# Kernel tuning notes

Hardware: AMD Instinct MI355X
Metric: run time of the kernel (lower is better)

Reference implementation:

```python
import jax, jax.numpy as jnp
import numpy as np

B, S, N, F, E, EF, H, L = 4, 16, 2048, 32, 16384, 8, 64, 2
H2 = H // 2


def setup_inputs() -> dict:
    key = jax.random.key(0)
    ks = iter(jax.random.split(key, 40))

    def g(shape, s=0.05):
        return jax.random.normal(next(ks), shape, jnp.float32) * s

    return dict(
        x=jax.random.normal(next(ks), (B, S, N, F), jnp.float32),
        edge_index=jax.random.randint(next(ks), (2, E), 0, N, dtype=jnp.int32),
        edge_attr=jax.random.normal(next(ks), (E, EF), jnp.float32),
        Wp=g((F, H)), bp=jnp.zeros((H,), jnp.float32),
        Wl=g((L, H, H)), bl=jnp.zeros((L, H), jnp.float32),
        Wr=g((L, H, H)), br=jnp.zeros((L, H), jnp.float32),
        We=g((L, EF, H)), att=g((L, H)), gb=jnp.zeros((L, H), jnp.float32),
        Wih=g((L, 3 * H, H)), Whh=g((L, 3 * H, H)),
        bih=jnp.zeros((L, 3 * H), jnp.float32), bhh=jnp.zeros((L, 3 * H), jnp.float32),
        oW1=g((H, H2)), ob1=jnp.zeros((H2,), jnp.float32),
        oW2=g((H2, 1)), ob2=jnp.zeros((1,), jnp.float32),
        dW1=g((H, H2)), db1=jnp.zeros((H2,), jnp.float32),
        dW2=g((H2, 1)), db2=jnp.zeros((1,), jnp.float32),
    )


def reference(x, edge_index, edge_attr, Wp, bp, Wl, bl, Wr, br, We, att, gb,
              Wih, Whh, bih, bhh, oW1, ob1, oW2, ob2, dW1, db1, dW2, db2):
    b, s, n, f = x.shape
    nl, _, h = Wl.shape
    src, dst = edge_index[0], edge_index[1]
    # GATv2Conv add_self_loops with fill_value='mean': self-loop attr = mean of
    # incoming edge attrs per destination node (0 if none).
    ones = jnp.ones((src.shape[0],), x.dtype)
    cnt = jax.ops.segment_sum(ones, dst, num_segments=n)
    loop_attr = jax.ops.segment_sum(edge_attr, dst, num_segments=n) / jnp.maximum(cnt, 1.0)[:, None]
    ar = jnp.arange(n, dtype=src.dtype)
    src_f = jnp.concatenate([src, ar])
    dst_f = jnp.concatenate([dst, ar])
    ea_f = jnp.concatenate([edge_attr, loop_attr], axis=0)  # [E2, EF]

    def gat(Xg, l):
        # Xg: [G, N, H] -- GATv2 (heads=1) applied independently per graph.
        XL = Xg @ Wl[l] + bl[l]
        XR = Xg @ Wr[l] + br[l]
        ep = ea_f @ We[l]                              # [E2, H]
        m = XL[:, src_f] + XR[:, dst_f] + ep[None]     # [G, E2, H]
        m = jax.nn.leaky_relu(m, 0.2)
        logits = m @ att[l]                            # [G, E2]
        seg_max = jax.vmap(lambda lg: jax.ops.segment_max(lg, dst_f, num_segments=n))(logits)
        p = jnp.exp(logits - seg_max[:, dst_f])
        den = jax.vmap(lambda pg: jax.ops.segment_sum(pg, dst_f, num_segments=n))(p)
        alpha = p / den[:, dst_f]
        out = jax.vmap(lambda a, xl: jax.ops.segment_sum(a[:, None] * xl[src_f], dst_f, num_segments=n))(alpha, XL)
        return out + gb[l]

    def gru(seq, l):
        # seq: [T, M, H]; PyTorch GRU gate order (r, z, n), scan over T.
        def step(hprev, xt):
            gi = xt @ Wih[l].T + bih[l]
            gh = hprev @ Whh[l].T + bhh[l]
            ir, iz, inn = jnp.split(gi, 3, -1)
            hr, hz, hn = jnp.split(gh, 3, -1)
            r = jax.nn.sigmoid(ir + hr)
            z = jax.nn.sigmoid(iz + hz)
            nn_ = jnp.tanh(inn + r * hn)
            hnew = (1.0 - z) * nn_ + z * hprev
            return hnew, hnew
        h0 = jnp.zeros(seq.shape[1:], seq.dtype)
        _, ys = jax.lax.scan(step, h0, seq)
        return ys

    X = x @ Wp + bp  # [B, S, N, H]
    for l in range(nl):
        # Original code applies GAT per (outer-t, inner-b) pair; the inner
        # TemporalGNN's GRU recurs over the BATCH axis (length B) per outer t.
        hg = gat(X.reshape(b * s, n, h), l).reshape(b, s, n, h)
        X = gru(hg.reshape(b, s * n, h), l).reshape(b, s, n, h)
    xl = X[:, -1].reshape(b * n, h)  # x[:, -1] then per-node heads, concat dim=1
    order = jax.nn.relu(xl @ oW1 + ob1) @ oW2 + ob2
    demand = jax.nn.relu(xl @ dW1 + db1) @ dW2 + db2
    return order[None], demand[None]  # each [1, B*N, 1]
```

## Files before the change

kernel.cpp:

```cpp
#include <hip/hip_runtime.h>
#include <math.h>

#define Bb   4
#define Ss   16
#define Nn   2048
#define Ff   32
#define Ee   16384
#define EFf  8
#define Hh   64
#define HB2  32
#define E2c  (Ee + Nn)
#define RTOT (Bb*Ss*Nn)
#define Mm   (Ss*Nn)
#define CST  68

typedef __attribute__((ext_vector_type(8))) short short8;
typedef __attribute__((ext_vector_type(4))) float f32x4;
#define MFMA16 __builtin_amdgcn_mfma_f32_16x16x32_bf16

__device__ __forceinline__ float sigf(float x) { return 1.f / (1.f + __expf(-x)); }
__device__ __forceinline__ float tanhfast(float x) { return 2.f / (1.f + __expf(-2.f * x)) - 1.f; }

__device__ __forceinline__ void split_bf16(float x, unsigned short& h, unsigned short& l) {
  unsigned u = __float_as_uint(x);
  unsigned r = (u + 0x7FFFu + ((u >> 16) & 1u)) >> 16;
  h = (unsigned short)r;
  float rest = x - __uint_as_float(r << 16);
  unsigned u2 = __float_as_uint(rest);
  l = (unsigned short)((u2 + 0x7FFFu + ((u2 >> 16) & 1u)) >> 16);
}

template <int PAT>
__device__ __forceinline__ float xorf(float v) {
  return __int_as_float(__builtin_amdgcn_ds_swizzle(__float_as_int(v), PAT));
}
__device__ __forceinline__ float red8(float v) {
  int x = __builtin_amdgcn_update_dpp(0, __float_as_int(v), 0x128, 0xF, 0xF, true);
  v += __int_as_float(x);
  v += xorf<0x401F>(v);
  v += __shfl_xor(v, 32, 64);
  return v;
}
__device__ __forceinline__ float redlogit(float v) {
  int x;
  x = __builtin_amdgcn_update_dpp(0, __float_as_int(v), 0xB1, 0xF, 0xF, true);
  v += __int_as_float(x);
  x = __builtin_amdgcn_update_dpp(0, __float_as_int(v), 0x4E, 0xF, 0xF, true);
  v += __int_as_float(x);
  v += xorf<0x101F>(v);
  return v;
}

__global__ __launch_bounds__(256) void k_loop_accum(
    const int* __restrict__ ei, const float* __restrict__ ea,
    float* __restrict__ cntF, float* __restrict__ loopA) {
  int idx = blockIdx.x * 256 + threadIdx.x;
  int e = idx >> 3, j = idx & 7;
  int d = ei[Ee + e];
  atomicAdd(&loopA[d * EFf + j], ea[idx]);
  if (j == 0) atomicAdd(&cntF[d], 1.0f);
}

__global__ __launch_bounds__(256) void k_scan(
    const float* __restrict__ cntF, int* __restrict__ offs) {
  __shared__ int partial[256];
  int tid = threadIdx.x;
  int base = tid * 8;
  int vals[8];
  int s = 0;
  for (int i = 0; i < 8; ++i) {
    int c = (int)cntF[base + i] + 1;
    vals[i] = c;
    s += c;
  }
  partial[tid] = s;
  __syncthreads();
  for (int off = 1; off < 256; off <<= 1) {
    int v = partial[tid];
    int add = (tid >= off) ? partial[tid - off] : 0;
    __syncthreads();
    partial[tid] = v + add;
    __syncthreads();
  }
  int run = (tid == 0) ? 0 : partial[tid - 1];
  for (int i = 0; i < 8; ++i) {
    offs[base + i] = run;
    run += vals[i];
  }
  if (tid == 255) offs[Nn] = run;
}

__global__ __launch_bounds__(256) void k_scatter(
    const int* __restrict__ ei, const int* __restrict__ offs,
    int* __restrict__ fillI, int* __restrict__ posOf, int* __restrict__ srcA) {
  int e = blockIdx.x * 256 + threadIdx.x;
  if (e >= E2c) return;
  int d = (e < Ee) ? ei[Ee + e] : (e - Ee);
  int s = (e < Ee) ? ei[e]      : (e - Ee);
  int pos = offs[d] + atomicAdd(&fillI[d], 1);
  posOf[e] = pos;
  srcA[pos] = s;
}

__global__ __launch_bounds__(256) void k_wprep(
    const float* __restrict__ Wl, const float* __restrict__ Wr,
    const float* __restrict__ Wih, const float* __restrict__ Whh,
    unsigned short* __restrict__ WXhi, unsigned short* __restrict__ WXlo,
    unsigned short* __restrict__ WGhi, unsigned short* __restrict__ WGlo) {
  int idx = blockIdx.x * 256 + threadIdx.x;
  if (idx < 16384) {
    int j = idx & 7, lane = (idx >> 3) & 63, kh = (idx >> 9) & 1;
    int t = (idx >> 10) & 7, l = idx >> 13;
    int n = t * 16 + (lane & 15);
    int k = kh * 32 + ((lane >> 4) << 3) + j;
    const float* W = (n < 64) ? (Wl + (size_t)l * 4096) : (Wr + (size_t)l * 4096);
    float v = W[k * 64 + (n & 63)];
    unsigned short h, lo;
    split_bf16(v, h, lo);
    WXhi[idx] = h; WXlo[idx] = lo;
  } else {
    int i2 = idx - 16384;
    int j = i2 & 7, lane = (i2 >> 3) & 63, kh = (i2 >> 9) & 1;
    int t = (i2 >> 10) % 24, l = i2 / 24576;
    int n = t * 16 + (lane & 15);
    int k = kh * 32 + ((lane >> 4) << 3) + j;
    int g = n >> 6, c = n & 63;
    const float* W = (g < 3) ? (Wih + (size_t)l * 12288 + (size_t)(g * 64 + c) * 64)
                             : (Whh + (size_t)l * 12288 + (size_t)((g - 3) * 64 + c) * 64);
    float v = W[k];
    unsigned short h, lo;
    split_bf16(v, h, lo);
    WGhi[i2] = h; WGlo[i2] = lo;
  }
}

__global__ __launch_bounds__(256) void k_ep(
    const float* __restrict__ ea, const float* __restrict__ loopA,
    const float* __restrict__ We, const int* __restrict__ posOf,
    const float* __restrict__ cntF, float* __restrict__ EPc) {
  __shared__ float wlds[EFf * Hh];
  int tid = threadIdx.x;
  int l = blockIdx.y;
  const float* Wel = We + (size_t)l * EFf * Hh;
  if (tid < EFf * Hh) wlds[tid] = Wel[tid];
  if (tid + 256 < EFf * Hh) wlds[tid + 256] = Wel[tid + 256];
  __syncthreads();
  int idx = blockIdx.x * 256 + tid;
  int e = idx >> 6, j = idx & 63;
  const float* a = (e < Ee) ? (ea + (size_t)e * EFf) : (loopA + (size_t)(e - Ee) * EFf);
  float acc = 0.f;
#pragma unroll
  for (int k = 0; k < EFf; ++k) acc += a[k] * wlds[k * Hh + j];
  if (e >= Ee) acc /= fmaxf(cntF[e - Ee], 1.0f);
  EPc[(size_t)l * E2c * Hh + (((size_t)posOf[e]) << 6) + j] = acc;
}

__global__ __launch_bounds__(256) void k_proj(
    const float* __restrict__ X, const float* __restrict__ Wp,
    const float* __restrict__ bp, float* __restrict__ Out) {
  __shared__ float w[32 * 16];
  int tid = threadIdx.x;
  int j0 = blockIdx.y << 4;
  for (int idx = tid; idx < 32 * 16; idx += 256)
    w[idx] = Wp[((idx >> 4) << 6) + j0 + (idx & 15)];
  __syncthreads();
  int r0 = (blockIdx.x << 9) + tid;
  float acc[2][16];
#pragma unroll
  for (int jj = 0; jj < 16; ++jj) { float b = bp[j0 + jj]; acc[0][jj] = b; acc[1][jj] = b; }
  const float* x0 = X + ((size_t)r0 << 5);
  const float* x1 = x0 + (256 << 5);
  for (int kc = 0; kc < 8; ++kc) {
    float4 a0 = *(const float4*)(x0 + 4 * kc);
    float4 a1 = *(const float4*)(x1 + 4 * kc);
    float a0a[4] = {a0.x, a0.y, a0.z, a0.w};
    float a1a[4] = {a1.x, a1.y, a1.z, a1.w};
#pragma unroll
    for (int q = 0; q < 4; ++q) {
      const float4* wp4 = (const float4*)(w + ((4 * kc + q) << 4));
#pragma unroll
      for (int q4 = 0; q4 < 4; ++q4) {
        float4 wv = wp4[q4];
        acc[0][4*q4+0] = fmaf(a0a[q], wv.x, acc[0][4*q4+0]);
        acc[0][4*q4+1] = fmaf(a0a[q], wv.y, acc[0][4*q4+1]);
        acc[0][4*q4+2] = fmaf(a0a[q], wv.z, acc[0][4*q4+2]);
        acc[0][4*q4+3] = fmaf(a0a[q], wv.w, acc[0][4*q4+3]);
        acc[1][4*q4+0] = fmaf(a1a[q], wv.x, acc[1][4*q4+0]);
        acc[1][4*q4+1] = fmaf(a1a[q], wv.y, acc[1][4*q4+1]);
        acc[1][4*q4+2] = fmaf(a1a[q], wv.z, acc[1][4*q4+2]);
        acc[1][4*q4+3] = fmaf(a1a[q], wv.w, acc[1][4*q4+3]);
      }
    }
  }
#pragma unroll
  for (int rr = 0; rr < 2; ++rr) {
    float* op = Out + (((size_t)(r0 + 256 * rr)) << 6) + j0;
#pragma unroll
    for (int q4 = 0; q4 < 4; ++q4)
      *(float4*)(op + 4 * q4) = make_float4(acc[rr][4*q4], acc[rr][4*q4+1], acc[rr][4*q4+2], acc[rr][4*q4+3]);
  }
}

__global__ __launch_bounds__(256) void k_xlr_mm(
    const float* __restrict__ X,
    const unsigned short* __restrict__ WXhi, const unsigned short* __restrict__ WXlo,
    const float* __restrict__ bl_, const float* __restrict__ br_,
    float* __restrict__ XL, float* __restrict__ XR) {
  __shared__ unsigned short ahi[4096], alo[4096];
  __shared__ float cbuf[64 * CST];
  int tid = threadIdx.x, lane = tid & 63, wv = tid >> 6;
  size_t m0 = (size_t)blockIdx.x << 6;
#pragma unroll
  for (int it = 0; it < 2; ++it) {
    int task = (it << 8) + tid;
    int row = task >> 3, cOct = task & 7;
    const float* src = X + ((m0 + row) << 6) + (cOct << 3);
    float4 a = *(const float4*)src;
    float4 b = *(const float4*)(src + 4);
    float va[8] = {a.x, a.y, a.z, a.w, b.x, b.y, b.z, b.w};
    short8 hv, lv;
#pragma unroll
    for (int j = 0; j < 8; ++j) {
      unsigned short hs, ls;
      split_bf16(va[j], hs, ls);
      hv[j] = (short)hs; lv[j] = (short)ls;
    }
    int f = ((cOct >> 2) * 4 + (row >> 4)) * 64 + ((cOct & 3) << 4) + (row & 15);
    *(short8*)&ahi[f << 3] = hv;
    *(short8*)&alo[f << 3] = lv;
  }
  __syncthreads();
  short8 Ah0 = *(const short8*)&ahi[((0 + wv) << 6 | lane) << 3];
  short8 Al0 = *(const short8*)&alo[((0 + wv) << 6 | lane) << 3];
  short8 Ah1 = *(const short8*)&ahi[((4 + wv) << 6 | lane) << 3];
  short8 Al1 = *(const short8*)&alo[((4 + wv) << 6 | lane) << 3];
  int nl = lane & 15;
  f32x4 acc[8];
#pragma unroll
  for (int t = 0; t < 8; ++t) {
    int n = t * 16 + nl;
    float b = (n < 64) ? bl_[n] : br_[n - 64];
    acc[t] = (f32x4){b, b, b, b};
  }
#pragma unroll
  for (int t = 0; t < 8; ++t) {
    const short8* bh0p = (const short8*)(WXhi + ((t << 1) << 9)) + lane;
    const short8* bl0p = (const short8*)(WXlo + ((t << 1) << 9)) + lane;
    const short8* bh1p = (const short8*)(WXhi + (((t << 1) + 1) << 9)) + lane;
    const short8* bl1p = (const short8*)(WXlo + (((t << 1) + 1) << 9)) + lane;
    short8 bh0 = *bh0p, bl0 = *bl0p, bh1 = *bh1p, bl1 = *bl1p;
    acc[t] = MFMA16(Ah0, bh0, acc[t], 0, 0, 0);
    acc[t] = MFMA16(Ah0, bl0, acc[t], 0, 0, 0);
    acc[t] = MFMA16(Al0, bh0, acc[t], 0, 0, 0);
    acc[t] = MFMA16(Ah1, bh1, acc[t], 0, 0, 0);
    acc[t] = MFMA16(Ah1, bl1, acc[t], 0, 0, 0);
    acc[t] = MFMA16(Al1, bh1, acc[t], 0, 0, 0);
  }
  int rbase = (wv << 4) + ((lane >> 4) << 2);
#pragma unroll
  for (int half = 0; half < 2; ++half) {
    __syncthreads();
#pragma unroll
    for (int tt = 0; tt < 4; ++tt) {
      int t = (half << 2) + tt;
#pragma unroll
      for (int reg = 0; reg < 4; ++reg)
        cbuf[(rbase + reg) * CST + (tt << 4) + nl] = acc[t][reg];
    }
    __syncthreads();
    float* dst = half ? XR : XL;
#pragma unroll
    for (int i = 0; i < 4; ++i) {
      int idx = (i << 10) + (tid << 2);
      int row = idx >> 6, col = idx & 63;
      *(float4*)(dst + ((m0 + row) << 6) + col) = *(float4*)&cbuf[row * CST + col];
    }
  }
}

__global__ __launch_bounds__(256) void k_gat(
    const float* __restrict__ XL, float* __restrict__ XR_HG,
    const float* __restrict__ EPc, const int* __restrict__ offs,
    const int* __restrict__ srcA,
    const float* __restrict__ att, const float* __restrict__ gbl) {
  int d = blockIdx.x;
  int q = blockIdx.y;
  int tid = threadIdx.x;
  int wv = tid >> 6, lane = tid & 63;
  int eSub = lane >> 3, hOct = lane & 7;
  int hb = hOct << 3;
  float at[8], gv[8];
  {
    float4 a0 = *(const float4*)(att + hb);
    float4 a1 = *(const float4*)(att + hb + 4);
    float4 g0v = *(const float4*)(gbl + hb);
    float4 g1v = *(const float4*)(gbl + hb + 4);
    at[0]=a0.x; at[1]=a0.y; at[2]=a0.z; at[3]=a0.w;
    at[4]=a1.x; at[5]=a1.y; at[6]=a1.z; at[7]=a1.w;
    gv[0]=g0v.x; gv[1]=g0v.y; gv[2]=g0v.z; gv[3]=g0v.w;
    gv[4]=g1v.x; gv[5]=g1v.y; gv[6]=g1v.z; gv[7]=g1v.w;
  }
  int p0 = offs[d], p1 = offs[d + 1];
  int nE = p1 - p0;
  int nCh = (nE + 7) >> 3;
  int gbase = (q << 4) + wv;
  size_t rowg[4];
  const float* Xg[4];
  float xr[4][8];
#pragma unroll
  for (int c = 0; c < 4; ++c) {
    int g = gbase + (c << 2);
    rowg[c] = ((size_t)(g * Nn + d)) << 6;
    Xg[c] = XL + (((size_t)g * Nn) << 6);
    float4 a = *(const float4*)(XR_HG + rowg[c] + hb);
    float4 b = *(const float4*)(XR_HG + rowg[c] + hb + 4);
    xr[c][0]=a.x; xr[c][1]=a.y; xr[c][2]=a.z; xr[c][3]=a.w;
    xr[c][4]=b.x; xr[c][5]=b.y; xr[c][6]=b.z; xr[c][7]=b.w;
  }
  float Sd[4] = {0.f, 0.f, 0.f, 0.f};
  float acc[4][8];
#pragma unroll
  for (int c = 0; c < 4; ++c)
#pragma unroll
    for (int j = 0; j < 8; ++j) acc[c][j] = 0.f;

  for (int ck = 0; ck < nCh; ++ck) {
    int p = (ck << 3) + eSub;
    int pc = p < nE ? p : nE - 1;
    int s = srcA[p0 + pc];
    const float* epp = EPc + (((size_t)(p0 + pc)) << 6) + hb;
    float4 e0 = *(const float4*)epp;
    float4 e1 = *(const float4*)(epp + 4);
    float ep[8] = {e0.x, e0.y, e0.z, e0.w, e1.x, e1.y, e1.z, e1.w};
    float xlv[4][8];
#pragma unroll
    for (int c = 0; c < 4; ++c) {
      const float* xp = Xg[c] + ((size_t)s << 6) + hb;
      float4 x0 = *(const float4*)xp;
      float4 x1 = *(const float4*)(xp + 4);
      xlv[c][0]=x0.x; xlv[c][1]=x0.y; xlv[c][2]=x0.z; xlv[c][3]=x0.w;
      xlv[c][4]=x1.x; xlv[c][5]=x1.y; xlv[c][6]=x1.z; xlv[c][7]=x1.w;
    }
    float v[4] = {0.f, 0.f, 0.f, 0.f};
#pragma unroll
    for (int c = 0; c < 4; ++c)
#pragma unroll
      for (int j = 0; j < 8; ++j) {
        float m = xlv[c][j] + xr[c][j] + ep[j];
        m = fmaxf(m, 0.2f * m);
        v[c] = fmaf(m, at[j], v[c]);
      }
#pragma unroll
    for (int c = 0; c < 4; ++c) v[c] = redlogit(v[c]);
    bool live = (p < nE);
#pragma unroll
    for (int c = 0; c < 4; ++c) {
      float w = live ? __expf(v[c]) : 0.f;
      Sd[c] += w;
#pragma unroll
      for (int j = 0; j < 8; ++j) acc[c][j] = fmaf(w, xlv[c][j], acc[c][j]);
    }
  }
#pragma unroll
  for (int c = 0; c < 4; ++c) {
    Sd[c] = red8(Sd[c]);
#pragma unroll
    for (int j = 0; j < 8; ++j) acc[c][j] = red8(acc[c][j]);
  }
  if (eSub == 0) {
#pragma unroll
    for (int c = 0; c < 4; ++c) {
      float inv = 1.f / Sd[c];
      float* op = XR_HG + rowg[c] + hb;
      *(float4*)(op)     = make_float4(fmaf(acc[c][0], inv, gv[0]), fmaf(acc[c][1], inv, gv[1]),
                                       fmaf(acc[c][2], inv, gv[2]), fmaf(acc[c][3], inv, gv[3]));
      *(float4*)(op + 4) = make_float4(fmaf(acc[c][4], inv, gv[4]), fmaf(acc[c][5], inv, gv[5]),
                                       fmaf(acc[c][6], inv, gv[6]), fmaf(acc[c][7], inv, gv[7]));
    }
  }
}

__device__ __forceinline__ void mm6l(f32x4& acc,
    short8 Ah0, short8 Al0, short8 Ah1, short8 Al1,
    const unsigned short* Whi, const unsigned short* Wlo,
    int tt, int lane) {
  const short8* bh0p = (const short8*)(Whi + (tt << 10)) + lane;
  const short8* bl0p = (const short8*)(Wlo + (tt << 10)) + lane;
  const short8* bh1p = (const short8*)(Whi + (tt << 10) + 512) + lane;
  const short8* bl1p = (const short8*)(Wlo + (tt << 10) + 512) + lane;
  short8 bh0 = *bh0p, bl0 = *bl0p, bh1 = *bh1p, bl1 = *bl1p;
  acc = MFMA16(Ah0, bh0, acc, 0, 0, 0);
  acc = MFMA16(Ah0, bl0, acc, 0, 0, 0);
  acc = MFMA16(Al0, bh0, acc, 0, 0, 0);
  acc = MFMA16(Ah1, bh1, acc, 0, 0, 0);
  acc = MFMA16(Ah1, bl1, acc, 0, 0, 0);
  acc = MFMA16(Al1, bh1, acc, 0, 0, 0);
}

__global__ __launch_bounds__(256) void k_gru_fused(
    const float* __restrict__ hgAll,
    const unsigned short* __restrict__ WGhi, const unsigned short* __restrict__ WGlo,
    const float* __restrict__ bih, const float* __restrict__ bhh,
    float* __restrict__ houtAll) {
  __shared__ unsigned short whi[24576], wlo[24576];
  __shared__ unsigned short ghi[4096], glo[4096];
  __shared__ float cbuf[64 * CST];
  int tid = threadIdx.x, lane = tid & 63, wv = tid >> 6;
  int nl = lane & 15;
  int rbase = (wv << 4) + ((lane >> 4) << 2);
  size_t m0 = (size_t)blockIdx.x << 6;

#pragma unroll
  for (int i = 0; i < 12; ++i) {
    int c = (i << 8) + tid;
    *(short8*)&whi[c << 3] = *(const short8*)(WGhi + ((size_t)c << 3));
    *(short8*)&wlo[c << 3] = *(const short8*)(WGlo + ((size_t)c << 3));
  }

  float biasR[4], biasZ[4], biasN[4], biasH[4];
#pragma unroll
  for (int ct = 0; ct < 4; ++ct) {
    int c = (ct << 4) + nl;
    biasR[ct] = bih[c]       + bhh[c];
    biasZ[ct] = bih[64 + c]  + bhh[64 + c];
    biasN[ct] = bih[128 + c];
    biasH[ct] = bhh[128 + c];
  }

  float4 pa[2], pb[2];
#pragma unroll
  for (int it = 0; it < 2; ++it) {
    int task = (it << 8) + tid;
    int row = task >> 3, cOct = task & 7;
    const float* srcg = hgAll + ((m0 + row) << 6) + (cOct << 3);
    pa[it] = *(const float4*)srcg;
    pb[it] = *(const float4*)(srcg + 4);
  }

  for (int t = 0; t < Bb; ++t) {
#pragma unroll
    for (int it = 0; it < 2; ++it) {
      int task = (it << 8) + tid;
      int row = task >> 3, cOct = task & 7;
      float va[8] = {pa[it].x, pa[it].y, pa[it].z, pa[it].w,
                     pb[it].x, pb[it].y, pb[it].z, pb[it].w};
      short8 hv8, lv8;
#pragma unroll
      for (int j = 0; j < 8; ++j) {
        unsigned short hs, ls;
        split_bf16(va[j], hs, ls);
        hv8[j] = (short)hs; lv8[j] = (short)ls;
      }
      int f = ((cOct >> 2) * 4 + (row >> 4)) * 64 + ((cOct & 3) << 4) + (row & 15);
      *(short8*)&ghi[f << 3] = hv8;
      *(short8*)&glo[f << 3] = lv8;
    }
    __syncthreads();

    short8 Gh0 = *(const short8*)&ghi[((0 + wv) << 6 | lane) << 3];
    short8 Gl0 = *(const short8*)&glo[((0 + wv) << 6 | lane) << 3];
    short8 Gh1 = *(const short8*)&ghi[((4 + wv) << 6 | lane) << 3];
    short8 Gl1 = *(const short8*)&glo[((4 + wv) << 6 | lane) << 3];

    if (t + 1 < Bb) {
      const float* hg = hgAll + (size_t)(t + 1) * ((size_t)Mm * Hh);
#pragma unroll
      for (int it = 0; it < 2; ++it) {
        int task = (it << 8) + tid;
        int row = task >> 3, cOct = task & 7;
        const float* srcg = hg + ((m0 + row) << 6) + (cOct << 3);
        pa[it] = *(const float4*)srcg;
        pb[it] = *(const float4*)(srcg + 4);
      }
    }

    short8 Ph0{}, Pl0{}, Ph1{}, Pl1{};
    if (t) {
      const float* cb = &cbuf[((wv << 4) + (lane & 15)) * CST + ((lane >> 4) << 3)];
      float4 p00 = *(const float4*)cb;
      float4 p01 = *(const float4*)(cb + 4);
      float4 p10 = *(const float4*)(cb + 32);
      float4 p11 = *(const float4*)(cb + 36);
      float v0[8] = {p00.x, p00.y, p00.z, p00.w, p01.x, p01.y, p01.z, p01.w};
      float v1[8] = {p10.x, p10.y, p10.z, p10.w, p11.x, p11.y, p11.z, p11.w};
#pragma unroll
      for (int j = 0; j < 8; ++j) {
        unsigned short hs, ls;
        split_bf16(v0[j], hs, ls);
        Ph0[j] = (short)hs; Pl0[j] = (short)ls;
        split_bf16(v1[j], hs, ls);
        Ph1[j] = (short)hs; Pl1[j] = (short)ls;
      }
    }

    f32x4 accR[4], accZ[4], accN[4], accH[4];
#pragma unroll
    for (int ct = 0; ct < 4; ++ct) {
      accR[ct] = (f32x4){biasR[ct], biasR[ct], biasR[ct], biasR[ct]};
      accZ[ct] = (f32x4){biasZ[ct], biasZ[ct], biasZ[ct], biasZ[ct]};
      accN[ct] = (f32x4){biasN[ct], biasN[ct], biasN[ct], biasN[ct]};
      accH[ct] = (f32x4){biasH[ct], biasH[ct], biasH[ct], biasH[ct]};
    }
#pragma unroll
    for (int ct = 0; ct < 4; ++ct) {
      mm6l(accR[ct], Gh0, Gl0, Gh1, Gl1, whi, wlo, 0 + ct, lane);
      mm6l(accZ[ct], Gh0, Gl0, Gh1, Gl1, whi, wlo, 4 + ct, lane);
      mm6l(accN[ct], Gh0, Gl0, Gh1, Gl1, whi, wlo, 8 + ct, lane);
    }
    if (t) {
#pragma unroll
      for (int ct = 0; ct < 4; ++ct) {
        mm6l(accR[ct], Ph0, Pl0, Ph1, Pl1, whi, wlo, 12 + ct, lane);
        mm6l(accZ[ct], Ph0, Pl0, Ph1, Pl1, whi, wlo, 16 + ct, lane);
        mm6l(accH[ct], Ph0, Pl0, Ph1, Pl1, whi, wlo, 20 + ct, lane);
      }
    }

#pragma unroll
    for (int ct = 0; ct < 4; ++ct) {
#pragma unroll
      for (int r = 0; r < 4; ++r) {
        float rgate = sigf(accR[ct][r]);
        float zg = sigf(accZ[ct][r]);
        float ng = tanhfast(accN[ct][r] + rgate * accH[ct][r]);
        int ci = (rbase + r) * CST + (ct << 4) + nl;
        float hp = t ? cbuf[ci] : 0.f;
        cbuf[ci] = (1.f - zg) * ng + zg * hp;
      }
    }
    __syncthreads();

    float* hout = houtAll + (size_t)t * ((size_t)Mm * Hh);
#pragma unroll
    for (int i = 0; i < 4; ++i) {
      int idx = (i << 10) + (tid << 2);
      int row = idx >> 6, col = idx & 63;
      *(float4*)(hout + ((m0 + row) << 6) + col) = *(float4*)&cbuf[row * CST + col];
    }
  }
}

__global__ __launch_bounds__(256) void k_heads(
    const float* __restrict__ Xb,
    const float* __restrict__ oW1, const float* __restrict__ ob1,
    const float* __restrict__ oW2, const float* __restrict__ ob2,
    const float* __restrict__ dW1, const float* __restrict__ db1,
    const float* __restrict__ dW2, const float* __restrict__ db2,
    float* __restrict__ out) {
  __shared__ float xa[64 * 65];
  __shared__ float w1o[64 * 32], w1d[64 * 32];
  __shared__ float po[4][64], pd[4][64];
  int tid = threadIdx.x;
  int rblk = blockIdx.x << 6;
  int b = rblk >> 11;
  int n0 = rblk & (Nn - 1);
  const float* src = Xb + (((size_t)b * Ss + (Ss - 1)) * Nn + n0) * Hh;
#pragma unroll
  for (int i = 0; i < 4; ++i) {
    int idx = (i << 10) + (tid << 2);
    int row = idx >> 6, col = idx & 63;
    float4 v = *(const float4*)(src + idx);
    float* dp = &xa[row * 65 + col];
    dp[0] = v.x; dp[1] = v.y; dp[2] = v.z; dp[3] = v.w;
  }
  for (int idx = tid; idx < 2048; idx += 256) {
    w1o[idx] = oW1[idx];
    w1d[idx] = dW1[idx];
  }
  __syncthreads();
  int row = tid & 63;
  int jg = tid >> 6;
  int j0 = jg << 3;
  float hO[8], hD[8];
#pragma unroll
  for (int j = 0; j < 8; ++j) { hO[j] = ob1[j0 + j]; hD[j] = db1[j0 + j]; }
  const float* xr = &xa[row * 65];
  for (int k = 0; k < 64; ++k) {
    float xv = xr[k];
    const float4* wo = (const float4*)&w1o[(k << 5) + j0];
    const float4* wd = (const float4*)&w1d[(k << 5) + j0];
    float4 o0 = wo[0], o1 = wo[1], d0 = wd[0], d1 = wd[1];
    hO[0] = fmaf(xv, o0.x, hO[0]); hO[1] = fmaf(xv, o0.y, hO[1]);
    hO[2] = fmaf(xv, o0.z, hO[2]); hO[3] = fmaf(xv, o0.w, hO[3]);
    hO[4] = fmaf(xv, o1.x, hO[4]); hO[5] = fmaf(xv, o1.y, hO[5]);
    hO[6] = fmaf(xv, o1.z, hO[6]); hO[7] = fmaf(xv, o1.w, hO[7]);
    hD[0] = fmaf(xv, d0.x, hD[0]); hD[1] = fmaf(xv, d0.y, hD[1]);
    hD[2] = fmaf(xv, d0.z, hD[2]); hD[3] = fmaf(xv, d0.w, hD[3]);
    hD[4] = fmaf(xv, d1.x, hD[4]); hD[5] = fmaf(xv, d1.y, hD[5]);
    hD[6] = fmaf(xv, d1.z, hD[6]); hD[7] = fmaf(xv, d1.w, hD[7]);
  }
  float accoP = 0.f, accdP = 0.f;
#pragma unroll
  for (int j = 0; j < 8; ++j) {
    accoP = fmaf(fmaxf(hO[j], 0.f), oW2[j0 + j], accoP);
    accdP = fmaf(fmaxf(hD[j], 0.f), dW2[j0 + j], accdP);
  }
  po[jg][row] = accoP;
  pd[jg][row] = accdP;
  __syncthreads();
  if (tid < 64) {
    int r = rblk + tid;
    out[r]           = ob2[0] + ((po[0][tid] + po[1][tid]) + (po[2][tid] + po[3][tid]));
    out[Bb * Nn + r] = db2[0] + ((pd[0][tid] + pd[1][tid]) + (pd[2][tid] + pd[3][tid]));
  }
}

extern "C" void kernel_launch(void* const* d_in, const int* in_sizes, int n_in,
                              void* d_out, int out_size, void* d_ws, size_t ws_size,
                              hipStream_t stream) {
  const float* x   = (const float*)d_in[0];
  const int*   ei  = (const int*)d_in[1];
  const float* ea  = (const float*)d_in[2];
  const float* Wp  = (const float*)d_in[3];
  const float* bp  = (const float*)d_in[4];
  const float* Wl  = (const float*)d_in[5];
  const float* bl  = (const float*)d_in[6];
  const float* Wr  = (const float*)d_in[7];
  const float* br  = (const float*)d_in[8];
  const float* We  = (const float*)d_in[9];
  const float* att = (const float*)d_in[10];
  const float* gb  = (const float*)d_in[11];
  const float* Wih = (const float*)d_in[12];
  const float* Whh = (const float*)d_in[13];
  const float* bih = (const float*)d_in[14];
  const float* bhh = (const float*)d_in[15];
  const float* oW1 = (const float*)d_in[16];
  const float* ob1 = (const float*)d_in[17];
  const float* oW2 = (const float*)d_in[18];
  const float* ob2 = (const float*)d_in[19];
  const float* dW1 = (const float*)d_in[20];
  const float* db1 = (const float*)d_in[21];
  const float* dW2 = (const float*)d_in[22];
  const float* db2 = (const float*)d_in[23];
  float* out = (float*)d_out;

  float* f    = (float*)d_ws;
  float* Xb   = f;
  float* XLb  = Xb  + (size_t)RTOT * Hh;
  float* XRb  = XLb + (size_t)RTOT * Hh;
  float* EPc  = XRb + (size_t)RTOT * Hh;
  unsigned short* WXhi = (unsigned short*)(EPc + (size_t)2 * E2c * Hh);
  unsigned short* WXlo = WXhi + 16384;
  unsigned short* WGhi = WXlo + 16384;
  unsigned short* WGlo = WGhi + 49152;
  float* cntF = (float*)(WGlo + 49152);
  float* loopA = cntF + Nn;
  int*   fillI = (int*)(loopA + Nn * EFf);
  int*   offs  = fillI + Nn;
  int*   posOf = offs + 2052;
  int*   srcA  = posOf + E2c;

  hipMemsetAsync(cntF, 0, (size_t)(Nn + Nn * EFf + Nn) * 4, stream);

  k_loop_accum<<<dim3(Ee * EFf / 256), 256, 0, stream>>>(ei, ea, cntF, loopA);
  k_scan<<<1, 256, 0, stream>>>(cntF, offs);
  k_scatter<<<dim3((E2c + 255) / 256), 256, 0, stream>>>(ei, offs, fillI, posOf, srcA);
  k_wprep<<<dim3(256), 256, 0, stream>>>(Wl, Wr, Wih, Whh, WXhi, WXlo, WGhi, WGlo);

  k_proj<<<dim3(RTOT / 512, 4), 256, 0, stream>>>(x, Wp, bp, Xb);

  k_ep<<<dim3(E2c * Hh / 256, 2), 256, 0, stream>>>(ea, loopA, We, posOf, cntF, EPc);

  for (int l = 0; l < 2; ++l) {
    k_xlr_mm<<<dim3(RTOT / 64), 256, 0, stream>>>(
        Xb, WXhi + (size_t)l * 8192, WXlo + (size_t)l * 8192,
        bl + (size_t)l * Hh, br + (size_t)l * Hh, XLb, XRb);
    k_gat<<<dim3(Nn, 4), 256, 0, stream>>>(
        XLb, XRb, EPc + (size_t)l * E2c * Hh, offs, srcA,
        att + (size_t)l * Hh, gb + (size_t)l * Hh);
    k_gru_fused<<<dim3(Mm / 64), 256, 0, stream>>>(
        XRb, WGhi + (size_t)l * 24576, WGlo + (size_t)l * 24576,
        bih + (size_t)l * 192, bhh + (size_t)l * 192, Xb);
  }

  k_heads<<<dim3(Bb * Nn / 64), 256, 0, stream>>>(
      Xb, oW1, ob1, oW2, ob2, dW1, db1, dW2, db2, out);
}
```

Measured before the change: 395.7 us.

## Hold GRU weight fragments in registers and split waves by output columns

```diff
diff --git a/kernel.cpp b/kernel.cpp
--- a/kernel.cpp
+++ b/kernel.cpp
@@ -380,15 +380,9 @@
   }
 }
 
-__device__ __forceinline__ void mm6l(f32x4& acc,
+__device__ __forceinline__ void mm6r(f32x4& acc,
     short8 Ah0, short8 Al0, short8 Ah1, short8 Al1,
-    const unsigned short* Whi, const unsigned short* Wlo,
-    int tt, int lane) {
-  const short8* bh0p = (const short8*)(Whi + (tt << 10)) + lane;
-  const short8* bl0p = (const short8*)(Wlo + (tt << 10)) + lane;
-  const short8* bh1p = (const short8*)(Whi + (tt << 10) + 512) + lane;
-  const short8* bl1p = (const short8*)(Wlo + (tt << 10) + 512) + lane;
-  short8 bh0 = *bh0p, bl0 = *bl0p, bh1 = *bh1p, bl1 = *bl1p;
+    short8 bh0, short8 bl0, short8 bh1, short8 bl1) {
   acc = MFMA16(Ah0, bh0, acc, 0, 0, 0);
   acc = MFMA16(Ah0, bl0, acc, 0, 0, 0);
   acc = MFMA16(Al0, bh0, acc, 0, 0, 0);
@@ -397,34 +391,35 @@
   acc = MFMA16(Al1, bh1, acc, 0, 0, 0);
 }
 
-__global__ __launch_bounds__(256) void k_gru_fused(
+__global__ __launch_bounds__(256, 2) void k_gru_fused(
     const float* __restrict__ hgAll,
     const unsigned short* __restrict__ WGhi, const unsigned short* __restrict__ WGlo,
     const float* __restrict__ bih, const float* __restrict__ bhh,
     float* __restrict__ houtAll) {
-  __shared__ unsigned short whi[24576], wlo[24576];
   __shared__ unsigned short ghi[4096], glo[4096];
   __shared__ float cbuf[64 * CST];
   int tid = threadIdx.x, lane = tid & 63, wv = tid >> 6;
   int nl = lane & 15;
-  int rbase = (wv << 4) + ((lane >> 4) << 2);
+  int rb0 = (lane >> 4) << 2;
   size_t m0 = (size_t)blockIdx.x << 6;
 
-#pragma unroll
-  for (int i = 0; i < 12; ++i) {
-    int c = (i << 8) + tid;
-    *(short8*)&whi[c << 3] = *(const short8*)(WGhi + ((size_t)c << 3));
-    *(short8*)&wlo[c << 3] = *(const short8*)(WGlo + ((size_t)c << 3));
-  }
-
-  float biasR[4], biasZ[4], biasN[4], biasH[4];
-#pragma unroll
-  for (int ct = 0; ct < 4; ++ct) {
-    int c = (ct << 4) + nl;
-    biasR[ct] = bih[c]       + bhh[c];
-    biasZ[ct] = bih[64 + c]  + bhh[64 + c];
-    biasN[ct] = bih[128 + c];
-    biasH[ct] = bhh[128 + c];
+  short8 Wh[6][2], Wl[6][2];
+#pragma unroll
+  for (int g = 0; g < 6; ++g) {
+    int tt = wv + (g << 2);
+    Wh[g][0] = *((const short8*)(WGhi + (tt << 10)) + lane);
+    Wh[g][1] = *((const short8*)(WGhi + (tt << 10) + 512) + lane);
+    Wl[g][0] = *((const short8*)(WGlo + (tt << 10)) + lane);
+    Wl[g][1] = *((const short8*)(WGlo + (tt << 10) + 512) + lane);
+  }
+
+  float biasR, biasZ, biasN, biasH;
+  {
+    int c = (wv << 4) + nl;
+    biasR = bih[c]       + bhh[c];
+    biasZ = bih[64 + c]  + bhh[64 + c];
+    biasN = bih[128 + c];
+    biasH = bhh[128 + c];
   }
 
   float4 pa[2], pb[2];
@@ -457,11 +452,6 @@
     }
     __syncthreads();
 
-    short8 Gh0 = *(const short8*)&ghi[((0 + wv) << 6 | lane) << 3];
-    short8 Gl0 = *(const short8*)&glo[((0 + wv) << 6 | lane) << 3];
-    short8 Gh1 = *(const short8*)&ghi[((4 + wv) << 6 | lane) << 3];
-    short8 Gl1 = *(const short8*)&glo[((4 + wv) << 6 | lane) << 3];
-
     if (t + 1 < Bb) {
       const float* hg = hgAll + (size_t)(t + 1) * ((size_t)Mm * Hh);
 #pragma unroll
@@ -474,56 +464,55 @@
       }
     }
 
-    short8 Ph0{}, Pl0{}, Ph1{}, Pl1{};
-    if (t) {
-      const float* cb = &cbuf[((wv << 4) + (lane & 15)) * CST + ((lane >> 4) << 3)];
-      float4 p00 = *(const float4*)cb;
-      float4 p01 = *(const float4*)(cb + 4);
-      float4 p10 = *(const float4*)(cb + 32);
-      float4 p11 = *(const float4*)(cb + 36);
-      float v0[8] = {p00.x, p00.y, p00.z, p00.w, p01.x, p01.y, p01.z, p01.w};
-      float v1[8] = {p10.x, p10.y, p10.z, p10.w, p11.x, p11.y, p11.z, p11.w};
-#pragma unroll
-      for (int j = 0; j < 8; ++j) {
-        unsigned short hs, ls;
-        split_bf16(v0[j], hs, ls);
-        Ph0[j] = (short)hs; Pl0[j] = (short)ls;
-        split_bf16(v1[j], hs, ls);
-        Ph1[j] = (short)hs; Pl1[j] = (short)ls;
+    f32x4 accR[4], accZ[4], accN[4], accH[4];
+#pragma unroll
+    for (int rg = 0; rg < 4; ++rg) {
+      accR[rg] = (f32x4){biasR, biasR, biasR, biasR};
+      accZ[rg] = (f32x4){biasZ, biasZ, biasZ, biasZ};
+      accN[rg] = (f32x4){biasN, biasN, biasN, biasN};
+      accH[rg] = (f32x4){biasH, biasH, biasH, biasH};
+    }
+#pragma unroll
+    for (int rg = 0; rg < 4; ++rg) {
+      short8 Gh0 = *(const short8*)&ghi[((0 + rg) << 6 | lane) << 3];
+      short8 Gl0 = *(const short8*)&glo[((0 + rg) << 6 | lane) << 3];
+      short8 Gh1 = *(const short8*)&ghi[((4 + rg) << 6 | lane) << 3];
+      short8 Gl1 = *(const short8*)&glo[((4 + rg) << 6 | lane) << 3];
+      mm6r(accR[rg], Gh0, Gl0, Gh1, Gl1, Wh[0][0], Wl[0][0], Wh[0][1], Wl[0][1]);
+      mm6r(accZ[rg], Gh0, Gl0, Gh1, Gl1, Wh[1][0], Wl[1][0], Wh[1][1], Wl[1][1]);
+      mm6r(accN[rg], Gh0, Gl0, Gh1, Gl1, Wh[2][0], Wl[2][0], Wh[2][1], Wl[2][1]);
+      if (t) {
+        const float* cb = &cbuf[((rg << 4) + (lane & 15)) * CST + ((lane >> 4) << 3)];
+        float4 p00 = *(const float4*)cb;
+        float4 p01 = *(const float4*)(cb + 4);
+        float4 p10 = *(const float4*)(cb + 32);
+        float4 p11 = *(const float4*)(cb + 36);
+        float v0[8] = {p00.x, p00.y, p00.z, p00.w, p01.x, p01.y, p01.z, p01.w};
+        float v1[8] = {p10.x, p10.y, p10.z, p10.w, p11.x, p11.y, p11.z, p11.w};
+        short8 Ph0, Pl0, Ph1, Pl1;
+#pragma unroll
+        for (int j = 0; j < 8; ++j) {
+          unsigned short hs, ls;
+          split_bf16(v0[j], hs, ls);
+          Ph0[j] = (short)hs; Pl0[j] = (short)ls;
+          split_bf16(v1[j], hs, ls);
+          Ph1[j] = (short)hs; Pl1[j] = (short)ls;
+        }
+        mm6r(accR[rg], Ph0, Pl0, Ph1, Pl1, Wh[3][0], Wl[3][0], Wh[3][1], Wl[3][1]);
+        mm6r(accZ[rg], Ph0, Pl0, Ph1, Pl1, Wh[4][0], Wl[4][0], Wh[4][1], Wl[4][1]);
+        mm6r(accH[rg], Ph0, Pl0, Ph1, Pl1, Wh[5][0], Wl[5][0], Wh[5][1], Wl[5][1]);
       }
     }
-
-    f32x4 accR[4], accZ[4], accN[4], accH[4];
-#pragma unroll
-    for (int ct = 0; ct < 4; ++ct) {
-      accR[ct] = (f32x4){biasR[ct], biasR[ct], biasR[ct], biasR[ct]};
-      accZ[ct] = (f32x4){biasZ[ct], biasZ[ct], biasZ[ct], biasZ[ct]};
-      accN[ct] = (f32x4){biasN[ct], biasN[ct], biasN[ct], biasN[ct]};
-      accH[ct] = (f32x4){biasH[ct], biasH[ct], biasH[ct], biasH[ct]};
-    }
-#pragma unroll
-    for (int ct = 0; ct < 4; ++ct) {
-      mm6l(accR[ct], Gh0, Gl0, Gh1, Gl1, whi, wlo, 0 + ct, lane);
-      mm6l(accZ[ct], Gh0, Gl0, Gh1, Gl1, whi, wlo, 4 + ct, lane);
-      mm6l(accN[ct], Gh0, Gl0, Gh1, Gl1, whi, wlo, 8 + ct, lane);
-    }
-    if (t) {
-#pragma unroll
-      for (int ct = 0; ct < 4; ++ct) {
-        mm6l(accR[ct], Ph0, Pl0, Ph1, Pl1, whi, wlo, 12 + ct, lane);
-        mm6l(accZ[ct], Ph0, Pl0, Ph1, Pl1, whi, wlo, 16 + ct, lane);
-        mm6l(accH[ct], Ph0, Pl0, Ph1, Pl1, whi, wlo, 20 + ct, lane);
-      }
-    }
-
-#pragma unroll
-    for (int ct = 0; ct < 4; ++ct) {
+    __syncthreads();
+
+#pragma unroll
+    for (int rg = 0; rg < 4; ++rg) {
 #pragma unroll
       for (int r = 0; r < 4; ++r) {
-        float rgate = sigf(accR[ct][r]);
-        float zg = sigf(accZ[ct][r]);
-        float ng = tanhfast(accN[ct][r] + rgate * accH[ct][r]);
-        int ci = (rbase + r) * CST + (ct << 4) + nl;
+        float rgate = sigf(accR[rg][r]);
+        float zg = sigf(accZ[rg][r]);
+        float ng = tanhfast(accN[rg][r] + rgate * accH[rg][r]);
+        int ci = ((rg << 4) + rb0 + r) * CST + (wv << 4) + nl;
         float hp = t ? cbuf[ci] : 0.f;
         cbuf[ci] = (1.f - zg) * ng + zg * hp;
       }
```

After: 375.9 us, median of 2. 5.0% less time.
